# Kernel optimization log

Measured on AMD Instinct MI355X. Metric: run time of the kernel, lower is better.

The kernel has to match this reference:

```python
import jax, jax.numpy as jnp
import numpy as np

H = 8      # heads
D = 64     # dim_head
DIM = 512  # model dim (== H*D)
LN_EPS = 1e-5


def setup_inputs() -> dict:
    key = jax.random.key(0)
    ks = jax.random.split(key, 4)
    B, N = 8, 1024
    x = jax.random.normal(ks[0], (B, N, DIM), dtype=jnp.float32)
    # params (torch Linear y = x @ W^T; we store W already transposed as (in, out))
    w_qkv = jax.random.normal(ks[1], (DIM, 3 * H * D), dtype=jnp.float32) * (DIM ** -0.5)
    w_out = jax.random.normal(ks[2], (H * D, DIM), dtype=jnp.float32) * ((H * D) ** -0.5)
    b_out = jnp.zeros((DIM,), dtype=jnp.float32)
    ln_g = jnp.ones((DIM,), dtype=jnp.float32)
    ln_b = jnp.zeros((DIM,), dtype=jnp.float32)
    return {"x": x, "w_qkv": w_qkv, "w_out": w_out, "b_out": b_out,
            "ln_g": ln_g, "ln_b": ln_b}


def reference(x, w_qkv, w_out, b_out, ln_g, ln_b):
    b, n, _ = x.shape
    qkv = x @ w_qkv                                   # [b, n, 3*H*D]
    q, k, v = jnp.split(qkv, 3, axis=-1)              # each [b, n, H*D]

    def to_heads(t):                                  # 'b n (h d) -> (b h) n d'
        return t.reshape(b, n, H, D).transpose(0, 2, 1, 3).reshape(b * H, n, D)

    q = to_heads(q)
    k = to_heads(k)
    v = to_heads(v)

    # FAITHFUL to source: k.view(b*h, -1, n) is a row-major reshape, NOT a
    # transpose, and NO scale is applied (self.scale is unused in forward).
    k_r = k.reshape(b * H, D, n)                      # [(bh), D, n] reinterpreted
    dots = jnp.matmul(q, k_r)                          # [(bh), n, n]
    attn = jax.nn.softmax(dots, axis=-1)
    out = jnp.matmul(attn, v)                          # [(bh), n, D]

    # '(b h) n d -> b n (h d)'
    out = out.reshape(b, H, n, D).transpose(0, 2, 1, 3).reshape(b, n, H * D)
    out = out @ w_out + b_out                          # to_out Linear (dropout=0)

    mu = jnp.mean(out, axis=-1, keepdims=True)
    var = jnp.var(out, axis=-1, keepdims=True)
    out = (out - mu) * jax.lax.rsqrt(var + LN_EPS) * ln_g + ln_b
    return out + x
```

## Files before the change

### kernel.cpp

```cpp
#include <hip/hip_runtime.h>

typedef unsigned short u16;
typedef unsigned int u32;
typedef __attribute__((ext_vector_type(4))) float f32x4;
typedef __attribute__((ext_vector_type(16))) float f32x16;
typedef __attribute__((ext_vector_type(8))) short s16x8;

__device__ __forceinline__ u16 bf16_rne(float f) {
    u32 u = __float_as_uint(f);
    u32 r = u + 0x7FFFu + ((u >> 16) & 1u);
    return (u16)(r >> 16);
}

__device__ __forceinline__ u32 cvt_pk_bf16(float lo, float hi) {
    u32 r;
    asm("v_cvt_pk_bf16_f32 %0, %1, %2" : "=v"(r) : "v"(lo), "v"(hi));
    return r;
}

__device__ __forceinline__ void gl_lds16(const void* g, void* l) {
    __builtin_amdgcn_global_load_lds(
        (const __attribute__((address_space(1))) u32*)g,
        (__attribute__((address_space(3))) u32*)l, 16, 0, 0);
}

#define MFMA16(a, b, c) __builtin_amdgcn_mfma_f32_16x16x32_bf16((a), (b), (c), 0, 0, 0)
#define MFMA32(a, b, c) __builtin_amdgcn_mfma_f32_32x32x16_bf16((a), (b), (c), 0, 0, 0)

union frag_u { u32 u[4]; s16x8 v; };

__global__ __launch_bounds__(256) void k_prep(const float* __restrict__ x,
                                              const float* __restrict__ w_qkv,
                                              const float* __restrict__ w_out,
                                              u16* __restrict__ xbf,
                                              u16* __restrict__ wqkvt,
                                              u16* __restrict__ woutt) {
    const int tid = threadIdx.x;
    if (blockIdx.x < 4096) {
        int i = blockIdx.x * 256 + tid;
        f32x4 v = *(const f32x4*)(x + (size_t)i * 4);
        u32* p = (u32*)(xbf + (size_t)i * 4);
        p[0] = cvt_pk_bf16(v.x, v.y);
        p[1] = cvt_pk_bf16(v.z, v.w);
        return;
    }
    __shared__ float tile[32][33];
    int idx = blockIdx.x - 4096;
    int bx_lin = idx & 63, by4 = idx >> 6;
    const float* in;
    u16* out;
    int C, bxc;
    if (bx_lin < 48) { in = w_qkv; out = wqkvt; C = 1536; bxc = bx_lin; }
    else             { in = w_out; out = woutt; C = 512;  bxc = bx_lin - 48; }
    const int R = 512;
    int bx = bxc * 32;
    int by = by4 * 32;
    int tx = tid & 31;
    int ty = tid >> 5;
#pragma unroll
    for (int i = 0; i < 32; i += 8)
        tile[ty + i][tx] = in[(size_t)(by + ty + i) * C + bx + tx];
    __syncthreads();
#pragma unroll
    for (int i = 0; i < 32; i += 8)
        out[(size_t)(bx + ty + i) * R + by + tx] = bf16_rne(tile[tx][ty + i]);
}

__global__ __launch_bounds__(256) void k_qkv_gemm(
    const u16* __restrict__ xbf, const u16* __restrict__ wt,
    u16* __restrict__ qh, u16* __restrict__ kRT, u16* __restrict__ vT) {
    __shared__ __align__(16) u16 lA[2][128 * 64];
    __shared__ __align__(16) u16 lB[2][128 * 64];
    const int tid = threadIdx.x;
    const int lane = tid & 63, l15 = lane & 15, l4 = lane >> 4;
    const int wid = tid >> 6, wm = wid >> 1, wn = wid & 1;
    const int hw = blockIdx.x;
    const int e = hw & 7, idx = hw >> 3;
    const int m0 = (e + 8 * (idx / 12)) * 128;
    const int c0 = (idx % 12) * 128;

    const char* gA = (const char*)xbf + (size_t)m0 * 1024;
    const char* gB = (const char*)wt + (size_t)c0 * 1024;
    const int srow = tid >> 3;
    const int scol = (tid & 7) * 16;

    const f32x4 z4 = {0.f, 0.f, 0.f, 0.f};
    f32x4 acc[4][4];
#pragma unroll
    for (int i = 0; i < 4; ++i)
#pragma unroll
        for (int j = 0; j < 4; ++j) acc[i][j] = z4;

    auto stage = [&](int buf, int kt) {
#pragma unroll
        for (int q = 0; q < 4; ++q) {
            int row = q * 32 + srow;
            int sc = scol ^ ((row & 7) << 4);
            gl_lds16(gA + (size_t)row * 1024 + kt * 128 + sc,
                     (char*)lA[buf] + q * 4096 + tid * 16);
            gl_lds16(gB + (size_t)row * 1024 + kt * 128 + sc,
                     (char*)lB[buf] + q * 4096 + tid * 16);
        }
    };

    stage(0, 0);
    __syncthreads();
    for (int kt = 0; kt < 8; ++kt) {
        int buf = kt & 1;
        if (kt < 7) stage(buf ^ 1, kt + 1);
        s16x8 af[4][2], bfr[4][2];
#pragma unroll
        for (int i = 0; i < 4; ++i)
#pragma unroll
            for (int k2 = 0; k2 < 2; ++k2) {
                int ra = wm * 64 + i * 16 + l15;
                int ca = (k2 * 64 + l4 * 16) ^ ((ra & 7) << 4);
                af[i][k2] = *(const s16x8*)((const char*)lA[buf] + ra * 128 + ca);
                int rb = wn * 64 + i * 16 + l15;
                int cb = (k2 * 64 + l4 * 16) ^ ((rb & 7) << 4);
                bfr[i][k2] = *(const s16x8*)((const char*)lB[buf] + rb * 128 + cb);
            }
        __builtin_amdgcn_s_setprio(1);
#pragma unroll
        for (int i = 0; i < 4; ++i)
#pragma unroll
            for (int j = 0; j < 4; ++j)
#pragma unroll
                for (int k2 = 0; k2 < 2; ++k2)
                    acc[i][j] = MFMA16(af[i][k2], bfr[j][k2], acc[i][j]);
        __builtin_amdgcn_s_setprio(0);
        __syncthreads();
    }

    char* ct = (char*)lA;
    const int which = c0 >> 9;
    const int hb = (c0 & 511) >> 6;
    const int b = m0 >> 10;
    const int n0 = m0 & 1023;
    const int i4 = (m0 >> 7) & 7;
    const float qsc = (which == 0) ? 1.4426950408889634f : 1.0f;

    if (which != 2) {
#pragma unroll
        for (int i = 0; i < 4; ++i)
#pragma unroll
            for (int j = 0; j < 4; ++j) {
                int col = wn * 64 + j * 16 + l15;
#pragma unroll
                for (int r = 0; r < 4; ++r) {
                    int rr = wm * 64 + i * 16 + l4 * 4 + r;
                    *(u16*)(ct + rr * 256 + ((col * 2) ^ ((rr & 7) << 4))) =
                        bf16_rne(acc[i][j][r] * qsc);
                }
            }
    } else {
#pragma unroll
        for (int i = 0; i < 4; ++i)
#pragma unroll
            for (int j = 0; j < 4; ++j) {
                int col = wn * 64 + j * 16 + l15;
#pragma unroll
                for (int r = 0; r < 4; ++r) {
                    int rr = wm * 64 + i * 16 + l4 * 4 + r;
                    *(u16*)(ct + col * 256 + ((rr * 2) ^ ((col & 7) << 4))) =
                        bf16_rne(acc[i][j][r]);
                }
            }
    }
    __syncthreads();

    if (which == 0) {
#pragma unroll
        for (int p = 0; p < 8; ++p) {
            int cid = p * 256 + tid;
            int row = cid >> 4, sub = cid & 15;
            s16x8 v = *(const s16x8*)(ct + row * 256 + ((sub * 16) ^ ((row & 7) << 4)));
            int bh = b * 8 + hb + (sub >> 3);
            *(s16x8*)((char*)qh + ((size_t)bh * 1024 + n0 + row) * 128 +
                      (sub & 7) * 16) = v;
        }
    } else if (which == 1) {
#pragma unroll
        for (int p = 0; p < 8; ++p) {
            int cid = p * 256 + tid;
            int h = cid >> 10, jb = (cid >> 6) & 15, jd = cid & 63;
            int colb = ((h * 64 + jd) * 2) ^ ((jb & 7) << 4);
            s16x8 v;
#pragma unroll
            for (int ii = 0; ii < 8; ++ii)
                v[ii] = *(const short*)(ct + (jb + ii * 16) * 256 + colb);
            int bh = b * 8 + hb + h;
            *(s16x8*)((char*)kRT + (size_t)bh * 131072 + jb * 8192 + i4 * 1024 +
                      jd * 16) = v;
        }
    } else {
#pragma unroll
        for (int p = 0; p < 8; ++p) {
            int cid = p * 256 + tid;
            int cl = cid >> 4, nc = cid & 15;
            s16x8 v = *(const s16x8*)(ct + cl * 256 + ((nc * 16) ^ ((cl & 7) << 4)));
            int bh = b * 8 + hb + (cl >> 6);
            *(s16x8*)((char*)vT + ((size_t)bh * 64 + (cl & 63)) * 2048 + n0 * 2 +
                      nc * 16) = v;
        }
    }
}

__global__ __launch_bounds__(256, 2) void k_attn(
    const u16* __restrict__ qh, const u16* __restrict__ kRT,
    const u16* __restrict__ vT, u16* __restrict__ attn_out) {
    __shared__ __align__(16) char smem[49152];
    char* qtile = smem;
    char* ktb = smem + 16384;
    char* vtb = smem + 32768;

    const int tid = threadIdx.x;
    const int lane = tid & 63, l31 = lane & 31, sg = lane >> 5;
    const int wv = tid >> 6;
    const int bh = blockIdx.x, mt = blockIdx.y;

    const char* kb = (const char*)kRT + (size_t)bh * 131072;
    const char* vb = (const char*)vT + (size_t)bh * 131072;
    const int srow = tid >> 3;
    const int scol = (tid & 7) * 16;

    {
        const char* gq = (const char*)qh + ((size_t)bh * 1024 + mt * 128) * 128;
#pragma unroll
        for (int q = 0; q < 4; ++q) {
            int row = q * 32 + srow;
            int sc = scol ^ ((row & 7) << 4);
            gl_lds16(gq + (size_t)row * 128 + sc, qtile + q * 4096 + tid * 16);
        }
#pragma unroll
        for (int q = 0; q < 2; ++q) {
            gl_lds16(kb + (q * 256 + tid) * 16, ktb + (q * 256 + tid) * 16);
            int row = q * 32 + srow;
            gl_lds16(vb + (size_t)row * 2048 + (scol ^ ((row & 7) << 4)),
                     vtb + q * 4096 + tid * 16);
        }
    }
    __syncthreads();

    const int qrow = wv * 32 + l31;
    s16x8 qf[4];
#pragma unroll
    for (int iq = 0; iq < 4; ++iq)
        qf[iq] = *(const s16x8*)(qtile + qrow * 128 +
                                 ((iq * 32 + sg * 16) ^ ((qrow & 7) << 4)));

    f32x16 zz;
#pragma unroll
    for (int r = 0; r < 16; ++r) zz[r] = 0.f;
    f32x16 o0 = zz, o1 = zz;
    float den = 0.f;

    for (int jb = 0; jb < 16; ++jb) {
        const int buf = jb & 1;
        if (jb < 15) {
            int nb = jb + 1, bufn = buf ^ 1;
#pragma unroll
            for (int q = 0; q < 2; ++q) {
                gl_lds16(kb + (size_t)nb * 8192 + (q * 256 + tid) * 16,
                         ktb + bufn * 8192 + (q * 256 + tid) * 16);
                int row = q * 32 + srow;
                gl_lds16(vb + (size_t)row * 2048 + nb * 128 +
                             (scol ^ ((row & 7) << 4)),
                         vtb + bufn * 8192 + q * 4096 + tid * 16);
            }
        }
        const char* kt = ktb + buf * 8192;
        const char* vt = vtb + buf * 8192;

        f32x16 s0 = zz, s1 = zz;
        __builtin_amdgcn_s_setprio(1);
#pragma unroll
        for (int iq = 0; iq < 4; ++iq) {
            const char* ka = kt + (2 * iq + sg) * 1024 + l31 * 16;
            s16x8 a0 = *(const s16x8*)(ka);
            s16x8 a1 = *(const s16x8*)(ka + 512);
            s0 = MFMA32(a0, qf[iq], s0);
            s1 = MFMA32(a1, qf[iq], s1);
        }
        __builtin_amdgcn_s_setprio(0);

        u32 u0[8], u1[8];
        {
            f32x16 e0, e1;
#pragma unroll
            for (int r = 0; r < 16; ++r) {
                e0[r] = exp2f(s0[r]);
                e1[r] = exp2f(s1[r]);
                den += e0[r] + e1[r];
            }
#pragma unroll
            for (int j = 0; j < 8; ++j) {
                u0[j] = cvt_pk_bf16(e0[2 * j], e0[2 * j + 1]);
                u1[j] = cvt_pk_bf16(e1[2 * j], e1[2 * j + 1]);
            }
        }
        s16x8 pa[4];
        {
            auto mix = [&](u32 lo, u32 hi, u32& wl, u32& wh) {
                u32 c = (u32)__shfl_xor((int)(sg ? lo : hi), 32);
                wl = sg ? c : lo;
                wh = sg ? hi : c;
            };
            frag_u f;
            mix(u0[0], u0[2], f.u[0], f.u[2]);
            mix(u0[1], u0[3], f.u[1], f.u[3]);
            pa[0] = f.v;
            mix(u0[4], u0[6], f.u[0], f.u[2]);
            mix(u0[5], u0[7], f.u[1], f.u[3]);
            pa[1] = f.v;
            mix(u1[0], u1[2], f.u[0], f.u[2]);
            mix(u1[1], u1[3], f.u[1], f.u[3]);
            pa[2] = f.v;
            mix(u1[4], u1[6], f.u[0], f.u[2]);
            mix(u1[5], u1[7], f.u[1], f.u[3]);
            pa[3] = f.v;
        }

        __builtin_amdgcn_s_setprio(1);
#pragma unroll
        for (int nq = 0; nq < 4; ++nq) {
            int cb = (nq * 32 + sg * 16) ^ ((l31 & 7) << 4);
            s16x8 v0 = *(const s16x8*)(vt + l31 * 128 + cb);
            s16x8 v1 = *(const s16x8*)(vt + (32 + l31) * 128 + cb);
            o0 = MFMA32(v0, pa[nq], o0);
            o1 = MFMA32(v1, pa[nq], o1);
        }
        __builtin_amdgcn_s_setprio(0);

        if (jb < 15) __syncthreads();
    }

    den += __shfl_xor(den, 32);
    float inv = 1.0f / den;

    {
        char* ow = smem + qrow * 128;
        int sw = (qrow & 7) << 4;
#pragma unroll
        for (int g = 0; g < 4; ++g) {
            uint2 w;
            w.x = cvt_pk_bf16(o0[4 * g] * inv, o0[4 * g + 1] * inv);
            w.y = cvt_pk_bf16(o0[4 * g + 2] * inv, o0[4 * g + 3] * inv);
            *(uint2*)(ow + ((16 * g + 8 * sg) ^ sw)) = w;
            w.x = cvt_pk_bf16(o1[4 * g] * inv, o1[4 * g + 1] * inv);
            w.y = cvt_pk_bf16(o1[4 * g + 2] * inv, o1[4 * g + 3] * inv);
            *(uint2*)(ow + ((64 + 16 * g + 8 * sg) ^ sw)) = w;
        }
    }
    __syncthreads();


    {
        char* dst = (char*)attn_out + ((size_t)(bh >> 3) * 1024 + mt * 128) * 1024 +
                    (bh & 7) * 128;
#pragma unroll
        for (int p = 0; p < 4; ++p) {
            int cid = p * 256 + tid;
            int row = cid >> 3, sub = cid & 7;
            s16x8 v = *(const s16x8*)(smem + row * 128 +
                                      ((sub * 16) ^ ((row & 7) << 4)));
            *(s16x8*)(dst + (size_t)row * 1024 + sub * 16) = v;
        }
    }
}

__global__ __launch_bounds__(512) void k_out_ln(
    const u16* __restrict__ aout, const u16* __restrict__ wt,
    const float* __restrict__ bias, const float* __restrict__ x,
    const float* __restrict__ g, const float* __restrict__ bb,
    float* __restrict__ out) {
    __shared__ __align__(16) char smem[131072];
    char* lB[2] = {smem, smem + 65536};
    const int tid = threadIdx.x;
    const int lane = tid & 63, l15 = lane & 15, l4 = lane >> 4;
    const int wid = tid >> 6, wm = wid >> 2, wn = wid & 3;
    const int m0 = blockIdx.x * 32;

    s16x8 af[16];
    {
        const char* arow = (const char*)aout + (size_t)(m0 + wm * 16 + l15) * 1024;
#pragma unroll
        for (int kk = 0; kk < 16; ++kk)
            af[kk] = *(const s16x8*)(arow + kk * 64 + l4 * 16);
    }

    auto stageB = [&](int buf, int kt) {
#pragma unroll
        for (int p = 0; p < 8; ++p) {
            int cid = p * 512 + tid;
            int n = cid >> 3, cc = cid & 7;
            int sc = (cc * 16) ^ ((n & 7) << 4);
            gl_lds16((const char*)wt + (size_t)n * 1024 + kt * 128 + sc,
                     lB[buf] + cid * 16);
        }
    };

    const f32x4 z4 = {0.f, 0.f, 0.f, 0.f};
    f32x4 acc[8];
#pragma unroll
    for (int j = 0; j < 8; ++j) acc[j] = z4;

    stageB(0, 0);
    __syncthreads();
    for (int kt = 0; kt < 8; ++kt) {
        int buf = kt & 1;
        if (kt < 7) stageB(buf ^ 1, kt + 1);
        s16x8 bf2[8][2];
#pragma unroll
        for (int j = 0; j < 8; ++j)
#pragma unroll
            for (int q = 0; q < 2; ++q) {
                int n = wn * 128 + j * 16 + l15;
                int cb = (q * 64 + l4 * 16) ^ ((n & 7) << 4);
                bf2[j][q] = *(const s16x8*)(lB[buf] + n * 128 + cb);
            }
        __builtin_amdgcn_s_setprio(1);
#pragma unroll
        for (int j = 0; j < 8; ++j)
#pragma unroll
            for (int q = 0; q < 2; ++q)
                acc[j] = MFMA16(af[kt * 2 + q], bf2[j][q], acc[j]);
        __builtin_amdgcn_s_setprio(0);
        __syncthreads();
    }

#pragma unroll
    for (int j = 0; j < 8; ++j) {
        int col = wn * 128 + j * 16 + l15;
        float bo = bias[col];
#pragma unroll
        for (int r = 0; r < 4; ++r) {
            int row = wm * 16 + l4 * 4 + r;
            *(float*)(smem + row * 2048 + ((col * 4) ^ ((row & 7) << 4))) =
                acc[j][r] + bo;
        }
    }
    __syncthreads();

    f32x4 g0 = *(const f32x4*)(g + lane * 8);
    f32x4 g1 = *(const f32x4*)(g + lane * 8 + 4);
    f32x4 b0 = *(const f32x4*)(bb + lane * 8);
    f32x4 b1 = *(const f32x4*)(bb + lane * 8 + 4);
#pragma unroll
    for (int rr = 0; rr < 4; ++rr) {
        int row = wid * 4 + rr;
        int sw = (row & 7) << 4;
        f32x4 v0 = *(const f32x4*)(smem + row * 2048 + ((lane * 32) ^ sw));
        f32x4 v1 = *(const f32x4*)(smem + row * 2048 + ((lane * 32 + 16) ^ sw));
        float s = v0.x + v0.y + v0.z + v0.w + v1.x + v1.y + v1.z + v1.w;
        float sq = v0.x * v0.x + v0.y * v0.y + v0.z * v0.z + v0.w * v0.w +
                   v1.x * v1.x + v1.y * v1.y + v1.z * v1.z + v1.w * v1.w;
#pragma unroll
        for (int m = 1; m < 64; m <<= 1) {
            s += __shfl_xor(s, m);
            sq += __shfl_xor(sq, m);
        }
        float mu = s * (1.0f / 512.0f);
        float var = sq * (1.0f / 512.0f) - mu * mu;
        float rstd = rsqrtf(var + 1e-5f);

        const float* xr = x + (size_t)(m0 + row) * 512 + lane * 8;
        f32x4 x0 = *(const f32x4*)(xr);
        f32x4 x1 = *(const f32x4*)(xr + 4);
        f32x4 r0, r1;
#pragma unroll
        for (int u = 0; u < 4; ++u) {
            r0[u] = (v0[u] - mu) * rstd * g0[u] + b0[u] + x0[u];
            r1[u] = (v1[u] - mu) * rstd * g1[u] + b1[u] + x1[u];
        }
        float* orow = out + (size_t)(m0 + row) * 512 + lane * 8;
        *(f32x4*)(orow) = r0;
        *(f32x4*)(orow + 4) = r1;
    }
}

extern "C" void kernel_launch(void* const* d_in, const int* in_sizes, int n_in,
                              void* d_out, int out_size, void* d_ws, size_t ws_size,
                              hipStream_t stream) {
    const float* x = (const float*)d_in[0];
    const float* w_qkv = (const float*)d_in[1];
    const float* w_out = (const float*)d_in[2];
    const float* b_out = (const float*)d_in[3];
    const float* ln_g = (const float*)d_in[4];
    const float* ln_b = (const float*)d_in[5];
    float* out = (float*)d_out;
    char* ws = (char*)d_ws;

    u16* xbf = (u16*)(ws + 0);
    u16* wqkvt = (u16*)(ws + 8388608);
    u16* woutt = (u16*)(ws + 9961472);
    u16* qh = (u16*)(ws + 10485760);
    u16* kRT = (u16*)(ws + 18874368);
    u16* vT = (u16*)(ws + 27262976);
    u16* aout = (u16*)(ws + 35651584);

    k_prep<<<5120, 256, 0, stream>>>(x, w_qkv, w_out, xbf, wqkvt, woutt);
    k_qkv_gemm<<<768, 256, 0, stream>>>(xbf, wqkvt, qh, kRT, vT);
    k_attn<<<dim3(64, 8), 256, 0, stream>>>(qh, kRT, vT, aout);
    k_out_ln<<<256, 512, 0, stream>>>(aout, woutt, b_out, x, ln_g, ln_b, out);
}
```

Measured before the change: 80.39 us.

## Halve attention block size to 64 query rows and double grid

The attention kernel now uses 128 threads covering 64 query rows per block, with a grid of 64x16 instead of 64x8, raising block count from 512 to 1024 to better fill the GPU's CUs. Q fragments are loaded directly from global memory into registers instead of being staged through LDS, which shrinks shared memory to 32KB. The cost is that each K/V tile is now loaded twice as often across blocks, raising L2 traffic. An extra barrier is added before the output tile reuses the K/V buffers.

```diff
diff --git a/kernel.cpp b/kernel.cpp
--- a/kernel.cpp
+++ b/kernel.cpp
@@ -206,13 +206,12 @@
     }
 }
 
-__global__ __launch_bounds__(256, 2) void k_attn(
+__global__ __launch_bounds__(128, 2) void k_attn(
     const u16* __restrict__ qh, const u16* __restrict__ kRT,
     const u16* __restrict__ vT, u16* __restrict__ attn_out) {
-    __shared__ __align__(16) char smem[49152];
-    char* qtile = smem;
-    char* ktb = smem + 16384;
-    char* vtb = smem + 32768;
+    __shared__ __align__(16) char smem[32768];
+    char* ktb = smem;
+    char* vtb = smem + 16384;
 
     const int tid = threadIdx.x;
     const int lane = tid & 63, l31 = lane & 31, sg = lane >> 5;
@@ -221,54 +220,41 @@
 
     const char* kb = (const char*)kRT + (size_t)bh * 131072;
     const char* vb = (const char*)vT + (size_t)bh * 131072;
-    const int srow = tid >> 3;
-    const int scol = (tid & 7) * 16;
-
-    {
-        const char* gq = (const char*)qh + ((size_t)bh * 1024 + mt * 128) * 128;
+
+    auto stageKV = [&](int buf, int jb) {
 #pragma unroll
         for (int q = 0; q < 4; ++q) {
-            int row = q * 32 + srow;
-            int sc = scol ^ ((row & 7) << 4);
-            gl_lds16(gq + (size_t)row * 128 + sc, qtile + q * 4096 + tid * 16);
-        }
-#pragma unroll
-        for (int q = 0; q < 2; ++q) {
-            gl_lds16(kb + (q * 256 + tid) * 16, ktb + (q * 256 + tid) * 16);
-            int row = q * 32 + srow;
-            gl_lds16(vb + (size_t)row * 2048 + (scol ^ ((row & 7) << 4)),
-                     vtb + q * 4096 + tid * 16);
-        }
-    }
-    __syncthreads();
+            int cid = q * 128 + tid;
+            gl_lds16(kb + (size_t)jb * 8192 + cid * 16, ktb + buf * 8192 + cid * 16);
+            int row = cid >> 3, sub = cid & 7;
+            gl_lds16(vb + (size_t)row * 2048 + jb * 128 +
+                         ((sub * 16) ^ ((row & 7) << 4)),
+                     vtb + buf * 8192 + cid * 16);
+        }
+    };
+
+    stageKV(0, 0);
 
     const int qrow = wv * 32 + l31;
     s16x8 qf[4];
-#pragma unroll
-    for (int iq = 0; iq < 4; ++iq)
-        qf[iq] = *(const s16x8*)(qtile + qrow * 128 +
-                                 ((iq * 32 + sg * 16) ^ ((qrow & 7) << 4)));
+    {
+        const char* gq = (const char*)qh +
+                         ((size_t)bh * 1024 + mt * 64 + qrow) * 128 + sg * 16;
+#pragma unroll
+        for (int iq = 0; iq < 4; ++iq)
+            qf[iq] = *(const s16x8*)(gq + iq * 32);
+    }
 
     f32x16 zz;
 #pragma unroll
     for (int r = 0; r < 16; ++r) zz[r] = 0.f;
     f32x16 o0 = zz, o1 = zz;
     float den = 0.f;
+    __syncthreads();
 
     for (int jb = 0; jb < 16; ++jb) {
         const int buf = jb & 1;
-        if (jb < 15) {
-            int nb = jb + 1, bufn = buf ^ 1;
-#pragma unroll
-            for (int q = 0; q < 2; ++q) {
-                gl_lds16(kb + (size_t)nb * 8192 + (q * 256 + tid) * 16,
-                         ktb + bufn * 8192 + (q * 256 + tid) * 16);
-                int row = q * 32 + srow;
-                gl_lds16(vb + (size_t)row * 2048 + nb * 128 +
-                             (scol ^ ((row & 7) << 4)),
-                         vtb + bufn * 8192 + q * 4096 + tid * 16);
-            }
-        }
+        if (jb < 15) stageKV(buf ^ 1, jb + 1);
         const char* kt = ktb + buf * 8192;
         const char* vt = vtb + buf * 8192;
 
@@ -338,6 +324,7 @@
     den += __shfl_xor(den, 32);
     float inv = 1.0f / den;
 
+    __syncthreads();
     {
         char* ow = smem + qrow * 128;
         int sw = (qrow & 7) << 4;
@@ -354,13 +341,12 @@
     }
     __syncthreads();
 
-
     {
-        char* dst = (char*)attn_out + ((size_t)(bh >> 3) * 1024 + mt * 128) * 1024 +
+        char* dst = (char*)attn_out + ((size_t)(bh >> 3) * 1024 + mt * 64) * 1024 +
                     (bh & 7) * 128;
 #pragma unroll
         for (int p = 0; p < 4; ++p) {
-            int cid = p * 256 + tid;
+            int cid = p * 128 + tid;
             int row = cid >> 3, sub = cid & 7;
             s16x8 v = *(const s16x8*)(smem + row * 128 +
                                       ((sub * 16) ^ ((row & 7) << 4)));
@@ -501,6 +487,6 @@
 
     k_prep<<<5120, 256, 0, stream>>>(x, w_qkv, w_out, xbf, wqkvt, woutt);
     k_qkv_gemm<<<768, 256, 0, stream>>>(xbf, wqkvt, qh, kRT, vT);
-    k_attn<<<dim3(64, 8), 256, 0, stream>>>(qh, kRT, vT, aout);
+    k_attn<<<dim3(64, 16), 128, 0, stream>>>(qh, kRT, vT, aout);
     k_out_ln<<<256, 512, 0, stream>>>(aout, woutt, b_out, x, ln_g, ln_b, out);
 }
```

Result: slower. 89.82 us (+11.7%).
